# Performance work log

Hardware: AMD Instinct MI355X
Metric: run time of the kernel (lower is better)

## Reference

```python
import jax, jax.numpy as jnp
import numpy as np

MARGIN = 0.2
EPS = 1e-6  # torch.pairwise_distance default eps added to (x1 - x2)


def setup_inputs() -> dict:
    key = jax.random.key(0)
    k1, k2 = jax.random.split(key)
    N, D = 8192, 128
    x = jax.random.normal(k1, (N, D), dtype=jnp.float32)
    target = jax.random.randint(k2, (N,), 0, 1000)
    return {"x": x, "target": target}


def _pairwise_dist(x):
    # torch.pairwise_distance(x.unsqueeze(0), x.unsqueeze(1)):
    #   diff[i, j] = x[j] - x[i] + EPS ; dist[i, j] = ||diff[i, j]||_2
    # Expanded quadratic form avoids the [N, N, D] diff tensor:
    #   ||a - b + e||^2 = ||a||^2 + ||b||^2 - 2 a.b + 2e*sum(a - b) + D*e^2
    sq = jnp.sum(x * x, axis=1)          # [N]
    s = jnp.sum(x, axis=1)               # [N]
    dot = x @ x.T                        # [N, N]
    D = x.shape[1]
    d2 = (sq[None, :] + sq[:, None] - 2.0 * dot
          + 2.0 * EPS * (s[None, :] - s[:, None]) + D * EPS * EPS)
    return jnp.sqrt(jnp.maximum(d2, 0.0))


def reference(x, target):
    N = x.shape[0]
    dist = _pairwise_dist(x)                                 # [N, N]
    same = target[None, :] == target[:, None]                # [N, N] bool
    pos_mask = (same & ~jnp.eye(N, dtype=bool)).astype(x.dtype)
    hardest_pos = jnp.max(pos_mask * dist, axis=1, keepdims=True)  # [N, 1]
    neg_mask = (~same).astype(x.dtype)
    max_neg = jnp.max(dist, axis=1, keepdims=True)           # [N, 1]
    anchor_neg = dist + max_neg * (1.0 - neg_mask)           # push positives up
    hardest_neg = jnp.min(anchor_neg, axis=1, keepdims=True) # [N, 1]
    loss = jax.nn.relu(hardest_pos - hardest_neg + MARGIN)
    return jnp.mean(loss)
```

## Files before the change

kernel.cpp:

```cpp
#include <hip/hip_runtime.h>

#define N 8192
#define Dk 128
#define EPSC 1e-6f
#define MARGIN 0.2f

typedef __attribute__((ext_vector_type(8))) short bf16x8;
typedef __attribute__((ext_vector_type(4))) float f32x4;

__device__ __forceinline__ unsigned short f2bf(float f) {
    unsigned u = __float_as_uint(f);
    u = (u + 0x7FFFu + ((u >> 16) & 1u)) >> 16;
    return (unsigned short)u;
}
__device__ __forceinline__ unsigned enc(float f) {
    unsigned u = __float_as_uint(f);
    return (u & 0x80000000u) ? ~u : (u | 0x80000000u);
}
__device__ __forceinline__ float dec(unsigned u) {
    return __uint_as_float((u & 0x80000000u) ? (u & 0x7FFFFFFFu) : ~u);
}

__device__ __forceinline__ void gl_lds16(const void* src, void* lds_dst) {
    __builtin_amdgcn_global_load_lds(
        (const __attribute__((address_space(1))) unsigned*)src,
        (__attribute__((address_space(3))) unsigned*)lds_dst, 16, 0, 0);
}

__global__ void prep_kernel(const float* __restrict__ x, const int* __restrict__ tgt,
                            unsigned short* __restrict__ XbA, unsigned short* __restrict__ XbB,
                            uint2* __restrict__ QT, float* __restrict__ P,
                            unsigned* __restrict__ wsHp, unsigned* __restrict__ wsMn) {
    int row = blockIdx.x * 4 + (threadIdx.x >> 6);
    int l = threadIdx.x & 63;
    const float2 v = *reinterpret_cast<const float2*>(&x[row * Dk + l * 2]);
    float sq = fmaf(v.x, v.x, v.y * v.y);
    float s = v.x + v.y;
    ushort2 a, b;
    a.x = f2bf(v.x);
    a.y = f2bf(v.y);
    b.x = f2bf(-2.0f * v.x);
    b.y = f2bf(-2.0f * v.y);
    int c_phys = (l >> 2) ^ (row & 7);
    int off = row * Dk + c_phys * 8 + 2 * (l & 3);
    *reinterpret_cast<ushort2*>(&XbA[off]) = a;
    *reinterpret_cast<ushort2*>(&XbB[off]) = b;
#pragma unroll
    for (int m = 32; m >= 1; m >>= 1) {
        sq += __shfl_xor(sq, m);
        s += __shfl_xor(s, m);
    }
    if (l == 0) {
        P[row] = sq - 2.0f * EPSC * s;
        uint2 qt;
        qt.x = __float_as_uint(sq + 2.0f * EPSC * s + (float)Dk * EPSC * EPSC);
        qt.y = (unsigned)tgt[row];
        QT[row] = qt;
        wsHp[row] = 0x007FFFFFu;
        wsMn[row] = 0xFF800000u;
    }
}

__global__ __launch_bounds__(256, 2) void main_kernel(
        const unsigned short* __restrict__ XbA, const unsigned short* __restrict__ XbB,
        const uint2* __restrict__ QT, const int* __restrict__ tgt,
        unsigned* __restrict__ wsHp, unsigned* __restrict__ wsMn) {
    __shared__ unsigned short Bs[128 * Dk];
    __shared__ uint2 QTs[128];

    const int tid = threadIdx.x;
    const int w = tid >> 6;
    const int lane = tid & 63;
    const int n = lane & 15;
    const int q = lane >> 4;
    const int wi = w >> 1;
    const int wj = w & 1;
    const int sw = n & 7;

    const int ig = (int)blockIdx.x >> 3;
    const int js = (int)blockIdx.x & 7;
    const int i0 = ig * 128;
    const int rbase = i0 + 64 * wi;

    bf16x8 Af[4][4];
#pragma unroll
    for (int ti = 0; ti < 4; ++ti) {
        const unsigned short* rp = &XbA[(rbase + 16 * ti + n) * Dk];
#pragma unroll
        for (int kk = 0; kk < 4; ++kk)
            Af[ti][kk] = *reinterpret_cast<const bf16x8*>(&rp[((q + 4 * kk) ^ sw) << 3]);
    }

    int tsl[16];
#pragma unroll
    for (int ti = 0; ti < 4; ++ti) {
        int4 t4 = *reinterpret_cast<const int4*>(&tgt[rbase + 16 * ti + 4 * q]);
        tsl[4 * ti + 0] = t4.x;
        tsl[4 * ti + 1] = t4.y;
        tsl[4 * ti + 2] = t4.z;
        tsl[4 * ti + 3] = t4.w;
    }

    float hp[16], mn[16];
#pragma unroll
    for (int s = 0; s < 16; ++s) {
        hp[s] = -INFINITY;
        mn[s] = INFINITY;
    }

    for (int step = 0; step < 8; ++step) {
        const int jbase = js * 1024 + step * 128;
        __syncthreads();
#pragma unroll
        for (int t = 0; t < 8; ++t) {
            const unsigned short* src = &XbB[(jbase + 32 * w + 4 * t) * Dk] + lane * 8;
            unsigned short* dst = &Bs[(32 * w + 4 * t) * Dk];
            gl_lds16(src, dst);
        }
        if (w == 0) {
            const unsigned short* src = reinterpret_cast<const unsigned short*>(&QT[jbase]) + lane * 8;
            gl_lds16(src, &QTs[0]);
        }
        __syncthreads();

        float Qv[4];
        int tv[4];
#pragma unroll
        for (int tj = 0; tj < 4; ++tj) {
            uint2 qt = QTs[64 * wj + 16 * tj + n];
            Qv[tj] = __uint_as_float(qt.x);
            tv[tj] = (int)qt.y;
        }

        f32x4 acc[4][4];
#pragma unroll
        for (int ti = 0; ti < 4; ++ti)
#pragma unroll
            for (int tj = 0; tj < 4; ++tj) acc[ti][tj] = Qv[tj];

#pragma unroll
        for (int kk = 0; kk < 4; ++kk) {
            bf16x8 Bf[4];
#pragma unroll
            for (int tj = 0; tj < 4; ++tj)
                Bf[tj] = *reinterpret_cast<const bf16x8*>(
                    &Bs[(64 * wj + 16 * tj + n) * Dk + (((q + 4 * kk) ^ sw) << 3)]);
#pragma unroll
            for (int ti = 0; ti < 4; ++ti)
#pragma unroll
                for (int tj = 0; tj < 4; ++tj)
                    acc[ti][tj] = __builtin_amdgcn_mfma_f32_16x16x32_bf16(Af[ti][kk], Bf[tj],
                                                                          acc[ti][tj], 0, 0, 0);
        }

#pragma unroll
        for (int tj = 0; tj < 4; ++tj) {
            int tvv = tv[tj];
#pragma unroll
            for (int ti = 0; ti < 4; ++ti) {
                f32x4 v = acc[ti][tj];
                int e0 = tvv == tsl[4 * ti + 0];
                int e1 = tvv == tsl[4 * ti + 1];
                int e2 = tvv == tsl[4 * ti + 2];
                int e3 = tvv == tsl[4 * ti + 3];
                if (__ballot(e0 | e1 | e2 | e3)) {
                    hp[4 * ti + 0] = fmaxf(hp[4 * ti + 0], e0 ? v[0] : -INFINITY);
                    hp[4 * ti + 1] = fmaxf(hp[4 * ti + 1], e1 ? v[1] : -INFINITY);
                    hp[4 * ti + 2] = fmaxf(hp[4 * ti + 2], e2 ? v[2] : -INFINITY);
                    hp[4 * ti + 3] = fmaxf(hp[4 * ti + 3], e3 ? v[3] : -INFINITY);
                    mn[4 * ti + 0] = fminf(mn[4 * ti + 0], e0 ? INFINITY : v[0]);
                    mn[4 * ti + 1] = fminf(mn[4 * ti + 1], e1 ? INFINITY : v[1]);
                    mn[4 * ti + 2] = fminf(mn[4 * ti + 2], e2 ? INFINITY : v[2]);
                    mn[4 * ti + 3] = fminf(mn[4 * ti + 3], e3 ? INFINITY : v[3]);
                } else {
                    mn[4 * ti + 0] = fminf(mn[4 * ti + 0], v[0]);
                    mn[4 * ti + 1] = fminf(mn[4 * ti + 1], v[1]);
                    mn[4 * ti + 2] = fminf(mn[4 * ti + 2], v[2]);
                    mn[4 * ti + 3] = fminf(mn[4 * ti + 3], v[3]);
                }
            }
        }
    }

#pragma unroll
    for (int m = 1; m <= 8; m <<= 1) {
#pragma unroll
        for (int s = 0; s < 16; ++s) {
            hp[s] = fmaxf(hp[s], __shfl_xor(hp[s], m));
            mn[s] = fminf(mn[s], __shfl_xor(mn[s], m));
        }
    }
    if (n == 0) {
#pragma unroll
        for (int ti = 0; ti < 4; ++ti) {
#pragma unroll
            for (int r = 0; r < 4; ++r) {
                int i = rbase + 16 * ti + 4 * q + r;
                atomicMax(&wsHp[i], enc(hp[4 * ti + r]));
                atomicMin(&wsMn[i], enc(mn[4 * ti + r]));
            }
        }
    }
}

__global__ void finish_kernel(const float* __restrict__ P,
                              const unsigned* __restrict__ wsHp,
                              const unsigned* __restrict__ wsMn,
                              float* __restrict__ out) {
    int t = threadIdx.x;
    float sum = 0.0f;
#pragma unroll
    for (int k = 0; k < 8; ++k) {
        int i = t + 1024 * k;
        float Pi = P[i];
        float hp = sqrtf(fmaxf(Pi + dec(wsHp[i]), 0.0f));
        float hn = sqrtf(fmaxf(Pi + dec(wsMn[i]), 0.0f));
        sum += fmaxf(hp - hn + MARGIN, 0.0f);
    }
#pragma unroll
    for (int m = 32; m >= 1; m >>= 1) sum += __shfl_xor(sum, m);
    __shared__ float ws[16];
    if ((t & 63) == 0) ws[t >> 6] = sum;
    __syncthreads();
    if (t == 0) {
        float tot = 0.0f;
#pragma unroll
        for (int i = 0; i < 16; ++i) tot += ws[i];
        out[0] = tot * (1.0f / (float)N);
    }
}

extern "C" void kernel_launch(void* const* d_in, const int* in_sizes, int n_in,
                              void* d_out, int out_size, void* d_ws, size_t ws_size,
                              hipStream_t stream) {
    const float* x = (const float*)d_in[0];
    const int* tgt = (const int*)d_in[1];
    float* out = (float*)d_out;

    char* ws = (char*)d_ws;
    const size_t xb = (size_t)N * Dk * 2;
    unsigned short* XbA = (unsigned short*)ws;
    unsigned short* XbB = (unsigned short*)(ws + xb);
    uint2* QT = (uint2*)(ws + 2 * xb);
    float* P = (float*)(ws + 2 * xb + (size_t)N * 8);
    unsigned* wsHp = (unsigned*)(ws + 2 * xb + (size_t)N * 12);
    unsigned* wsMn = (unsigned*)(ws + 2 * xb + (size_t)N * 16);

    prep_kernel<<<N / 4, 256, 0, stream>>>(x, tgt, XbA, XbB, QT, P, wsHp, wsMn);
    main_kernel<<<512, 256, 0, stream>>>(XbA, XbB, QT, tgt, wsHp, wsMn);
    finish_kernel<<<1, 1024, 0, stream>>>(P, wsHp, wsMn, out);
}
```

Baseline: 98.32 us.

## Drop LDS staging of B tile and reuse single bf16 matrix for both operands

Removes the shared-memory staging of the B operand and QT, so each wave loads B fragments and QT entries straight from global memory (relying on L1/L2) and the per-step block barriers go away. Keeps one unswizzled bf16 copy of x instead of separate A and -2x copies. To make that work, the -2 scale is folded out: accumulators start at -Q/2, dot products are accumulated directly, min/max roles are swapped, and the finish kernel multiplies by -2. This cuts prep writes and removes barriers, at the cost of redundant global/L2 traffic for B between the two wi waves and possibly less coalesced fragment loads.

```diff
diff --git a/kernel.cpp b/kernel.cpp
--- a/kernel.cpp
+++ b/kernel.cpp
@@ -21,30 +21,19 @@
     return __uint_as_float((u & 0x80000000u) ? (u & 0x7FFFFFFFu) : ~u);
 }
 
-__device__ __forceinline__ void gl_lds16(const void* src, void* lds_dst) {
-    __builtin_amdgcn_global_load_lds(
-        (const __attribute__((address_space(1))) unsigned*)src,
-        (__attribute__((address_space(3))) unsigned*)lds_dst, 16, 0, 0);
-}
-
 __global__ void prep_kernel(const float* __restrict__ x, const int* __restrict__ tgt,
-                            unsigned short* __restrict__ XbA, unsigned short* __restrict__ XbB,
-                            uint2* __restrict__ QT, float* __restrict__ P,
+                            unsigned short* __restrict__ Xb, uint2* __restrict__ QT,
+                            float* __restrict__ P,
                             unsigned* __restrict__ wsHp, unsigned* __restrict__ wsMn) {
     int row = blockIdx.x * 4 + (threadIdx.x >> 6);
     int l = threadIdx.x & 63;
     const float2 v = *reinterpret_cast<const float2*>(&x[row * Dk + l * 2]);
     float sq = fmaf(v.x, v.x, v.y * v.y);
     float s = v.x + v.y;
-    ushort2 a, b;
+    ushort2 a;
     a.x = f2bf(v.x);
     a.y = f2bf(v.y);
-    b.x = f2bf(-2.0f * v.x);
-    b.y = f2bf(-2.0f * v.y);
-    int c_phys = (l >> 2) ^ (row & 7);
-    int off = row * Dk + c_phys * 8 + 2 * (l & 3);
-    *reinterpret_cast<ushort2*>(&XbA[off]) = a;
-    *reinterpret_cast<ushort2*>(&XbB[off]) = b;
+    *reinterpret_cast<ushort2*>(&Xb[row * Dk + l * 2]) = a;
 #pragma unroll
     for (int m = 32; m >= 1; m >>= 1) {
         sq += __shfl_xor(sq, m);
@@ -52,22 +41,20 @@
     }
     if (l == 0) {
         P[row] = sq - 2.0f * EPSC * s;
+        float Qj = sq + 2.0f * EPSC * s + (float)Dk * EPSC * EPSC;
         uint2 qt;
-        qt.x = __float_as_uint(sq + 2.0f * EPSC * s + (float)Dk * EPSC * EPSC);
+        qt.x = __float_as_uint(-0.5f * Qj);
         qt.y = (unsigned)tgt[row];
         QT[row] = qt;
-        wsHp[row] = 0x007FFFFFu;
-        wsMn[row] = 0xFF800000u;
+        wsHp[row] = 0xFF800000u;
+        wsMn[row] = 0x007FFFFFu;
     }
 }
 
 __global__ __launch_bounds__(256, 2) void main_kernel(
-        const unsigned short* __restrict__ XbA, const unsigned short* __restrict__ XbB,
+        const unsigned short* __restrict__ Xb,
         const uint2* __restrict__ QT, const int* __restrict__ tgt,
         unsigned* __restrict__ wsHp, unsigned* __restrict__ wsMn) {
-    __shared__ unsigned short Bs[128 * Dk];
-    __shared__ uint2 QTs[128];
-
     const int tid = threadIdx.x;
     const int w = tid >> 6;
     const int lane = tid & 63;
@@ -75,21 +62,19 @@
     const int q = lane >> 4;
     const int wi = w >> 1;
     const int wj = w & 1;
-    const int sw = n & 7;
 
     const int ig = (int)blockIdx.x >> 3;
     const int js = (int)blockIdx.x & 7;
-    const int i0 = ig * 128;
-    const int rbase = i0 + 64 * wi;
+    const int rbase = ig * 128 + 64 * wi;
+
+    const bf16x8* Xv = reinterpret_cast<const bf16x8*>(Xb);
 
     bf16x8 Af[4][4];
 #pragma unroll
-    for (int ti = 0; ti < 4; ++ti) {
-        const unsigned short* rp = &XbA[(rbase + 16 * ti + n) * Dk];
+    for (int ti = 0; ti < 4; ++ti)
 #pragma unroll
         for (int kk = 0; kk < 4; ++kk)
-            Af[ti][kk] = *reinterpret_cast<const bf16x8*>(&rp[((q + 4 * kk) ^ sw) << 3]);
-    }
+            Af[ti][kk] = Xv[(rbase + 16 * ti + n) * 16 + (q + 4 * kk)];
 
     int tsl[16];
 #pragma unroll
@@ -104,30 +89,18 @@
     float hp[16], mn[16];
 #pragma unroll
     for (int s = 0; s < 16; ++s) {
-        hp[s] = -INFINITY;
-        mn[s] = INFINITY;
+        hp[s] = INFINITY;
+        mn[s] = -INFINITY;
     }
 
     for (int step = 0; step < 8; ++step) {
         const int jbase = js * 1024 + step * 128;
-        __syncthreads();
-#pragma unroll
-        for (int t = 0; t < 8; ++t) {
-            const unsigned short* src = &XbB[(jbase + 32 * w + 4 * t) * Dk] + lane * 8;
-            unsigned short* dst = &Bs[(32 * w + 4 * t) * Dk];
-            gl_lds16(src, dst);
-        }
-        if (w == 0) {
-            const unsigned short* src = reinterpret_cast<const unsigned short*>(&QT[jbase]) + lane * 8;
-            gl_lds16(src, &QTs[0]);
-        }
-        __syncthreads();
 
         float Qv[4];
         int tv[4];
 #pragma unroll
         for (int tj = 0; tj < 4; ++tj) {
-            uint2 qt = QTs[64 * wj + 16 * tj + n];
+            uint2 qt = QT[jbase + 64 * wj + 16 * tj + n];
             Qv[tj] = __uint_as_float(qt.x);
             tv[tj] = (int)qt.y;
         }
@@ -143,8 +116,7 @@
             bf16x8 Bf[4];
 #pragma unroll
             for (int tj = 0; tj < 4; ++tj)
-                Bf[tj] = *reinterpret_cast<const bf16x8*>(
-                    &Bs[(64 * wj + 16 * tj + n) * Dk + (((q + 4 * kk) ^ sw) << 3)]);
+                Bf[tj] = Xv[(jbase + 64 * wj + 16 * tj + n) * 16 + (q + 4 * kk)];
 #pragma unroll
             for (int ti = 0; ti < 4; ++ti)
 #pragma unroll
@@ -164,19 +136,19 @@
                 int e2 = tvv == tsl[4 * ti + 2];
                 int e3 = tvv == tsl[4 * ti + 3];
                 if (__ballot(e0 | e1 | e2 | e3)) {
-                    hp[4 * ti + 0] = fmaxf(hp[4 * ti + 0], e0 ? v[0] : -INFINITY);
-                    hp[4 * ti + 1] = fmaxf(hp[4 * ti + 1], e1 ? v[1] : -INFINITY);
-                    hp[4 * ti + 2] = fmaxf(hp[4 * ti + 2], e2 ? v[2] : -INFINITY);
-                    hp[4 * ti + 3] = fmaxf(hp[4 * ti + 3], e3 ? v[3] : -INFINITY);
-                    mn[4 * ti + 0] = fminf(mn[4 * ti + 0], e0 ? INFINITY : v[0]);
-                    mn[4 * ti + 1] = fminf(mn[4 * ti + 1], e1 ? INFINITY : v[1]);
-                    mn[4 * ti + 2] = fminf(mn[4 * ti + 2], e2 ? INFINITY : v[2]);
-                    mn[4 * ti + 3] = fminf(mn[4 * ti + 3], e3 ? INFINITY : v[3]);
+                    hp[4 * ti + 0] = fminf(hp[4 * ti + 0], e0 ? v[0] : INFINITY);
+                    hp[4 * ti + 1] = fminf(hp[4 * ti + 1], e1 ? v[1] : INFINITY);
+                    hp[4 * ti + 2] = fminf(hp[4 * ti + 2], e2 ? v[2] : INFINITY);
+                    hp[4 * ti + 3] = fminf(hp[4 * ti + 3], e3 ? v[3] : INFINITY);
+                    mn[4 * ti + 0] = fmaxf(mn[4 * ti + 0], e0 ? -INFINITY : v[0]);
+                    mn[4 * ti + 1] = fmaxf(mn[4 * ti + 1], e1 ? -INFINITY : v[1]);
+                    mn[4 * ti + 2] = fmaxf(mn[4 * ti + 2], e2 ? -INFINITY : v[2]);
+                    mn[4 * ti + 3] = fmaxf(mn[4 * ti + 3], e3 ? -INFINITY : v[3]);
                 } else {
-                    mn[4 * ti + 0] = fminf(mn[4 * ti + 0], v[0]);
-                    mn[4 * ti + 1] = fminf(mn[4 * ti + 1], v[1]);
-                    mn[4 * ti + 2] = fminf(mn[4 * ti + 2], v[2]);
-                    mn[4 * ti + 3] = fminf(mn[4 * ti + 3], v[3]);
+                    mn[4 * ti + 0] = fmaxf(mn[4 * ti + 0], v[0]);
+                    mn[4 * ti + 1] = fmaxf(mn[4 * ti + 1], v[1]);
+                    mn[4 * ti + 2] = fmaxf(mn[4 * ti + 2], v[2]);
+                    mn[4 * ti + 3] = fmaxf(mn[4 * ti + 3], v[3]);
                 }
             }
         }
@@ -186,8 +158,8 @@
     for (int m = 1; m <= 8; m <<= 1) {
 #pragma unroll
         for (int s = 0; s < 16; ++s) {
-            hp[s] = fmaxf(hp[s], __shfl_xor(hp[s], m));
-            mn[s] = fminf(mn[s], __shfl_xor(mn[s], m));
+            hp[s] = fminf(hp[s], __shfl_xor(hp[s], m));
+            mn[s] = fmaxf(mn[s], __shfl_xor(mn[s], m));
         }
     }
     if (n == 0) {
@@ -196,8 +168,8 @@
 #pragma unroll
             for (int r = 0; r < 4; ++r) {
                 int i = rbase + 16 * ti + 4 * q + r;
-                atomicMax(&wsHp[i], enc(hp[4 * ti + r]));
-                atomicMin(&wsMn[i], enc(mn[4 * ti + r]));
+                atomicMin(&wsHp[i], enc(hp[4 * ti + r]));
+                atomicMax(&wsMn[i], enc(mn[4 * ti + r]));
             }
         }
     }
@@ -213,8 +185,8 @@
     for (int k = 0; k < 8; ++k) {
         int i = t + 1024 * k;
         float Pi = P[i];
-        float hp = sqrtf(fmaxf(Pi + dec(wsHp[i]), 0.0f));
-        float hn = sqrtf(fmaxf(Pi + dec(wsMn[i]), 0.0f));
+        float hp = sqrtf(fmaxf(fmaf(-2.0f, dec(wsHp[i]), Pi), 0.0f));
+        float hn = sqrtf(fmaxf(fmaf(-2.0f, dec(wsMn[i]), Pi), 0.0f));
         sum += fmaxf(hp - hn + MARGIN, 0.0f);
     }
 #pragma unroll
@@ -239,14 +211,13 @@
 
     char* ws = (char*)d_ws;
     const size_t xb = (size_t)N * Dk * 2;
-    unsigned short* XbA = (unsigned short*)ws;
-    unsigned short* XbB = (unsigned short*)(ws + xb);
-    uint2* QT = (uint2*)(ws + 2 * xb);
-    float* P = (float*)(ws + 2 * xb + (size_t)N * 8);
-    unsigned* wsHp = (unsigned*)(ws + 2 * xb + (size_t)N * 12);
-    unsigned* wsMn = (unsigned*)(ws + 2 * xb + (size_t)N * 16);
-
-    prep_kernel<<<N / 4, 256, 0, stream>>>(x, tgt, XbA, XbB, QT, P, wsHp, wsMn);
-    main_kernel<<<512, 256, 0, stream>>>(XbA, XbB, QT, tgt, wsHp, wsMn);
+    unsigned short* Xb = (unsigned short*)ws;
+    uint2* QT = (uint2*)(ws + xb);
+    float* P = (float*)(ws + xb + (size_t)N * 8);
+    unsigned* wsHp = (unsigned*)(ws + xb + (size_t)N * 12);
+    unsigned* wsMn = (unsigned*)(ws + xb + (size_t)N * 16);
+
+    prep_kernel<<<N / 4, 256, 0, stream>>>(x, tgt, Xb, QT, P, wsHp, wsMn);
+    main_kernel<<<512, 256, 0, stream>>>(Xb, QT, tgt, wsHp, wsMn);
     finish_kernel<<<1, 1024, 0, stream>>>(P, wsHp, wsMn, out);
 }
```

Result: slower. 110.9 us (+12.8%).
